# Kernel tuning notes

Measured on AMD Instinct MI355X. Metric: run time of the kernel, lower is better.

Reference implementation:

```python
import jax, jax.numpy as jnp
import numpy as np

N = 50000        # nodes
E = 800000       # edges (avg degree 16)
NODE_D = 128     # node_attr_dim
EDGE_D = 16      # edge_attr_dim
HID = 300        # hidden_dim (module default)


def setup_inputs() -> dict:
    key = jax.random.key(0)
    ks = jax.random.split(key, 8)
    x = jax.random.normal(ks[0], (N, NODE_D), jnp.float32)
    edge_attr = jax.random.normal(ks[1], (E, EDGE_D), jnp.float32)
    edge_weight = jax.random.uniform(ks[2], (E,), jnp.float32)
    node_weight = jax.random.uniform(ks[3], (N,), jnp.float32)
    edge_index = jax.random.randint(ks[4], (2, E), 0, N, jnp.int32)
    # lin0: Linear(node_attr_dim + edge_attr_dim, hidden_dim)
    W0 = jax.random.normal(ks[5], (NODE_D + EDGE_D, HID), jnp.float32) / np.sqrt(NODE_D + EDGE_D)
    b0 = jnp.zeros((HID,), jnp.float32)
    # mp_layer.linear: Linear(hidden_dim, hidden_dim)
    W = jax.random.normal(ks[6], (HID, HID), jnp.float32) / np.sqrt(HID)
    b = jnp.zeros((HID,), jnp.float32)
    return dict(x=x, edge_attr=edge_attr, edge_weight=edge_weight,
                node_weight=node_weight, W0=W0, b0=b0, W=W, b=b,
                edge_index=edge_index)


def reference(x, edge_attr, edge_weight, node_weight, W0, b0, W, b, edge_index):
    src = edge_index[0]   # x_j (source, flow='source_to_target')
    dst = edge_index[1]   # aggregation target i
    n = x.shape[0]

    # --- isFirstLayer: weighted sum of incoming edge features, scattered at dst ---
    inc = jax.ops.segment_sum(edge_weight[:, None] * edge_attr, dst, num_segments=n)  # [N, EDGE_D]
    h0 = jax.nn.relu(jnp.concatenate([x, inc], axis=1) @ W0 + b0)                     # [N, HID]

    # --- MessagePassingLayer: message = edge_weight * x_j; aggr = mean at dst ---
    msg = edge_weight[:, None] * h0[src]                                              # [E, HID]
    agg = jax.ops.segment_sum(msg, dst, num_segments=n)                               # [N, HID]
    deg = jax.ops.segment_sum(jnp.ones((src.shape[0],), x.dtype), dst, num_segments=n)
    agg = agg / jnp.maximum(deg, 1.0)[:, None]  # scatter-mean (0 where no incoming edges)

    # --- update: relu(h0 + linear(aggr)) (add_residual=True) ---
    h = jax.nn.relu(h0 + agg @ W + b)
    # isLastLayer=False -> no node_weight scaling
    return (h, h0)
```

## Files before the change

kernel.cpp:

```cpp
#include <hip/hip_runtime.h>

#define NN 50000
#define NE 800000
#define ND 128
#define ED 16
#define HID 300
#define KP1 192
#define KP2 320
#define NP 320

#define SCAN_T 256
#define SCAN_B ((NN + SCAN_T - 1) / SCAN_T)

typedef __attribute__((ext_vector_type(8))) short short8;
typedef __attribute__((ext_vector_type(4))) float f32x4;

__device__ __forceinline__ unsigned short f2b(float f) {
    unsigned int u = __float_as_uint(f);
    u = (u + 0x7FFFu + ((u >> 16) & 1u)) >> 16;
    return (unsigned short)u;
}
__device__ __forceinline__ float blo(unsigned int u) {
    return __uint_as_float(u << 16);
}
__device__ __forceinline__ float bhi(unsigned int u) {
    return __uint_as_float(u & 0xffff0000u);
}

__device__ __forceinline__ void gload16(const void* g, void* l) {
    __builtin_amdgcn_global_load_lds(
        (const __attribute__((address_space(1))) void*)g,
        (__attribute__((address_space(3))) void*)l, 16, 0, 0);
}

__device__ __forceinline__ int block_iscan(int v, int tid) {
    int lane = tid & 63;
    #pragma unroll
    for (int off = 1; off < 64; off <<= 1) {
        int t = __shfl_up(v, off);
        if (lane >= off) v += t;
    }
    __shared__ int wsum[4];
    int wid = tid >> 6;
    if (lane == 63) wsum[wid] = v;
    __syncthreads();
    int add = 0;
    #pragma unroll
    for (int w = 0; w < 4; ++w)
        if (w < wid) add += wsum[w];
    return v + add;
}

__global__ void hist_kernel(const int* __restrict__ ei, int* __restrict__ rowptr) {
    int e = blockIdx.x * blockDim.x + threadIdx.x;
    if (e < NE) atomicAdd(&rowptr[ei[NE + e] + 1], 1);
}

__global__ __launch_bounds__(SCAN_T) void scan1(int* __restrict__ rowptr,
                                                int* __restrict__ blockSums) {
    int i = blockIdx.x * SCAN_T + threadIdx.x;
    int v = (i < NN) ? rowptr[1 + i] : 0;
    v = block_iscan(v, threadIdx.x);
    if (i < NN) rowptr[1 + i] = v;
    if (threadIdx.x == SCAN_T - 1) blockSums[blockIdx.x] = v;
}

__global__ __launch_bounds__(SCAN_T) void scan2(int* __restrict__ blockSums) {
    int t = threadIdx.x;
    int orig = (t < SCAN_B) ? blockSums[t] : 0;
    int v = block_iscan(orig, t);
    if (t < SCAN_B) blockSums[t] = v - orig;
}

__global__ __launch_bounds__(SCAN_T) void scan3(int* __restrict__ rowptr,
                                                const int* __restrict__ blockSums,
                                                int* __restrict__ cursor) {
    int i = blockIdx.x * SCAN_T + threadIdx.x;
    if (i < NN) {
        int v = rowptr[1 + i] + blockSums[blockIdx.x];
        rowptr[1 + i] = v;
        if (i + 1 < NN) cursor[i + 1] = v;
    }
    if (i == 0) cursor[0] = 0;
}

__global__ void fill_kernel(const int* __restrict__ ei, const float* __restrict__ ew,
                            int* __restrict__ cursor, uint4* __restrict__ csr) {
    int e = blockIdx.x * blockDim.x + threadIdx.x;
    if (e < NE) {
        int d = ei[NE + e];
        int pos = atomicAdd(&cursor[d], 1);
        uint4 q;
        q.x = (unsigned int)ei[e];
        q.y = (unsigned int)e;
        q.z = __float_as_uint(ew[e]);
        q.w = 0;
        csr[pos] = q;
    }
}

__global__ __launch_bounds__(256) void prep_kernel(
    const float* __restrict__ x,
    const float* __restrict__ edge_attr,
    const int* __restrict__ rowptr,
    const uint4* __restrict__ csr,
    unsigned short* __restrict__ A1) {
    int n = (blockIdx.x * blockDim.x + threadIdx.x) >> 6;
    int lane = threadIdx.x & 63;
    if (n >= NN) return;

    float2 v = *(const float2*)&x[(size_t)n * ND + lane * 2];
    unsigned int o = (unsigned int)f2b(v.x) | ((unsigned int)f2b(v.y) << 16);
    *(unsigned int*)&A1[(size_t)n * KP1 + lane * 2] = o;

    int g = lane >> 4, j = lane & 15;
    int lo = rowptr[n], hi = rowptr[n + 1];
    float s = 0.f;
    for (int k = lo + g; k < hi; k += 8) {
        int k1 = (k + 4 < hi) ? k + 4 : k;
        uint4 e0 = csr[k];
        uint4 e1 = csr[k1];
        float a0 = edge_attr[(size_t)e0.y * ED + j];
        float a1 = edge_attr[(size_t)e1.y * ED + j];
        s += __uint_as_float(e0.z) * a0;
        s += ((k + 4 < hi) ? __uint_as_float(e1.z) : 0.f) * a1;
    }
    s += __shfl_xor(s, 16);
    s += __shfl_xor(s, 32);
    if (lane < 16)
        A1[(size_t)n * KP1 + ND + lane] = f2b(s);
    else
        A1[(size_t)n * KP1 + ND + lane] = 0;
}

__global__ void castB0(const float* __restrict__ W0, unsigned short* __restrict__ B0T) {
    int n = blockIdx.x, k = threadIdx.x;
    float v = (n < HID && k < ND + ED) ? W0[(size_t)k * HID + n] : 0.f;
    B0T[(size_t)n * KP1 + k] = f2b(v);
}

__global__ void castB(const float* __restrict__ W, unsigned short* __restrict__ BT) {
    int n = blockIdx.x, k = threadIdx.x;
    float v = (n < HID && k < HID) ? W[(size_t)k * HID + n] : 0.f;
    BT[(size_t)n * KP2 + k] = f2b(v);
}

template <int MODE, int KP, int BN, int WM, int WN, int RPB>
__global__ __launch_bounds__(256) void gemm_stream(
    const unsigned short* __restrict__ A,
    const unsigned short* __restrict__ BT,
    const float* __restrict__ bias,
    const float* __restrict__ RES,
    float* __restrict__ C,
    unsigned short* __restrict__ h0b,
    int M)
{
    constexpr int CPR = KP / 8;
    constexpr int ACH = 32 * CPR;
    constexpr int BCH = BN * CPR;
    constexpr int AM  = 32 / (16 * WM);
    constexpr int BNW = BN / (16 * WN);
    __shared__ unsigned short Bs[BCH * 8];
    __shared__ unsigned short As[2][ACH * 8];

    const int tid = threadIdx.x;
    const int wave = tid >> 6, lane = tid & 63;
    const int wm = wave / WN, wn = wave % WN;
    const int quad = lane >> 4, lr = lane & 15;
    const int n00 = blockIdx.y * BN;
    const int rbase = blockIdx.x * RPB;
    const int rowend = min(rbase + RPB, M);
    const int nt = (rowend - rbase + 31) >> 5;

    #pragma unroll
    for (int rd = 0; rd < BCH / 256; ++rd) {
        int s = rd * 256 + tid;
        int row = s / CPR, c = s - row * CPR;
        int cs = (c & ~7) | ((c & 7) ^ (row & 7));
        gload16(&BT[(size_t)(n00 + row) * KP + cs * 8], &Bs[s * 8]);
    }
    auto stageA = [&](int buf, int mb) {
        #pragma unroll
        for (int rd = 0; rd < ACH / 256; ++rd) {
            int s = rd * 256 + tid;
            int row = s / CPR, c = s - row * CPR;
            int cs = (c & ~7) | ((c & 7) ^ (row & 7));
            int mg = mb + row; if (mg >= M) mg = M - 1;
            gload16(&A[(size_t)mg * KP + cs * 8], &As[buf][s * 8]);
        }
    };
    stageA(0, rbase);

    float bias_r[BNW];
    #pragma unroll
    for (int tn = 0; tn < BNW; ++tn) {
        int ng = n00 + wn * (BNW * 16) + tn * 16 + lr;
        bias_r[tn] = (ng < HID) ? bias[ng] : 0.f;
    }
    __syncthreads();

    int cur = 0;
    #pragma unroll 1
    for (int t = 0; t < nt; ++t) {
        const int mb = rbase + t * 32;
        if (t + 1 < nt) stageA(cur ^ 1, mb + 32);

        float res_r[AM][BNW][4];
        if (MODE == 1) {
            #pragma unroll
            for (int tm = 0; tm < AM; ++tm)
            #pragma unroll
            for (int tn = 0; tn < BNW; ++tn) {
                int ng = n00 + wn * (BNW * 16) + tn * 16 + lr;
                int ngc = ng < HID ? ng : HID - 1;
                #pragma unroll
                for (int r = 0; r < 4; ++r) {
                    int mg = mb + (wm * AM + tm) * 16 + quad * 4 + r;
                    int mgc = mg < M ? mg : M - 1;
                    res_r[tm][tn][r] = RES[(size_t)mgc * HID + ngc];
                }
            }
        }

        f32x4 acc[AM][BNW] = {};
        const int rm = lr & 7;
        #pragma unroll
        for (int tt = 0; tt < KP / 32; ++tt) {
            int cA = tt * 4 + quad;
            int sw8 = ((cA & ~7) | ((cA & 7) ^ rm)) * 8;
            short8 a[AM], b[BNW];
            #pragma unroll
            for (int tm = 0; tm < AM; ++tm) {
                int ar = (wm * AM + tm) * 16 + lr;
                a[tm] = *(const short8*)&As[cur][ar * KP + sw8];
            }
            #pragma unroll
            for (int tn = 0; tn < BNW; ++tn) {
                int br = wn * (BNW * 16) + tn * 16 + lr;
                b[tn] = *(const short8*)&Bs[br * KP + sw8];
            }
            #pragma unroll
            for (int tm = 0; tm < AM; ++tm)
                #pragma unroll
                for (int tn = 0; tn < BNW; ++tn)
                    acc[tm][tn] = __builtin_amdgcn_mfma_f32_16x16x32_bf16(
                        a[tm], b[tn], acc[tm][tn], 0, 0, 0);
        }

        #pragma unroll
        for (int tm = 0; tm < AM; ++tm)
        #pragma unroll
        for (int tn = 0; tn < BNW; ++tn) {
            int ng = n00 + wn * (BNW * 16) + tn * 16 + lr;
            #pragma unroll
            for (int r = 0; r < 4; ++r) {
                int mg = mb + (wm * AM + tm) * 16 + quad * 4 + r;
                if (mg < rowend && ng < HID) {
                    float v = acc[tm][tn][r] + bias_r[tn];
                    if (MODE == 1) v += res_r[tm][tn][r];
                    v = fmaxf(v, 0.f);
                    C[(size_t)mg * HID + ng] = v;
                    if (MODE == 0) h0b[(size_t)mg * NP + ng] = f2b(v);
                }
            }
        }
        __syncthreads();
        cur ^= 1;
    }
}

__device__ __forceinline__ void acc8(float* acc, float w, const uint4& r) {
    acc[0] += w * blo(r.x); acc[1] += w * bhi(r.x);
    acc[2] += w * blo(r.y); acc[3] += w * bhi(r.y);
    acc[4] += w * blo(r.z); acc[5] += w * bhi(r.z);
    acc[6] += w * blo(r.w); acc[7] += w * bhi(r.w);
}

__global__ __launch_bounds__(256) void agg_kernel(
    const unsigned short* __restrict__ h0b,
    const int* __restrict__ rowptr,
    const uint4* __restrict__ csr,
    unsigned short* __restrict__ aggB)
{
    int n = (blockIdx.x * blockDim.x + threadIdx.x) >> 6;
    int lane = threadIdx.x & 63;
    if (n >= NN) return;
    int lo = rowptr[n], hi = rowptr[n + 1];
    float acc[8] = {};
    const uint4* h4 = (const uint4*)h0b;
    bool act = lane < 40;
    for (int k = lo; k < hi; k += 4) {
        int k1 = (k + 1 < hi) ? k + 1 : k;
        int k2 = (k + 2 < hi) ? k + 2 : k;
        int k3 = (k + 3 < hi) ? k + 3 : k;
        uint4 p0 = csr[k], p1 = csr[k1], p2 = csr[k2], p3 = csr[k3];
        float w0 = __uint_as_float(p0.z);
        float w1 = (k + 1 < hi) ? __uint_as_float(p1.z) : 0.f;
        float w2 = (k + 2 < hi) ? __uint_as_float(p2.z) : 0.f;
        float w3 = (k + 3 < hi) ? __uint_as_float(p3.z) : 0.f;
        uint4 r0 = {0,0,0,0}, r1 = {0,0,0,0}, r2 = {0,0,0,0}, r3 = {0,0,0,0};
        if (act) {
            r0 = h4[(size_t)p0.x * 40 + lane];
            r1 = h4[(size_t)p1.x * 40 + lane];
            r2 = h4[(size_t)p2.x * 40 + lane];
            r3 = h4[(size_t)p3.x * 40 + lane];
        }
        acc8(acc, w0, r0);
        acc8(acc, w1, r1);
        acc8(acc, w2, r2);
        acc8(acc, w3, r3);
    }
    if (act) {
        float invd = 1.f / fmaxf((float)(hi - lo), 1.f);
        int cbase = lane * 8;
        unsigned int o[4];
        #pragma unroll
        for (int i = 0; i < 4; ++i) {
            int c0 = cbase + 2 * i, c1 = c0 + 1;
            unsigned int ulo = (c0 < HID) ? f2b(acc[2 * i] * invd) : 0;
            unsigned int uhi = (c1 < HID) ? f2b(acc[2 * i + 1] * invd) : 0;
            o[i] = ulo | (uhi << 16);
        }
        uint4* a4 = (uint4*)aggB;
        uint4 v; v.x = o[0]; v.y = o[1]; v.z = o[2]; v.w = o[3];
        a4[(size_t)n * 40 + lane] = v;
    }
}

extern "C" void kernel_launch(void* const* d_in, const int* in_sizes, int n_in,
                              void* d_out, int out_size, void* d_ws, size_t ws_size,
                              hipStream_t stream) {
    const float* x           = (const float*)d_in[0];
    const float* edge_attr   = (const float*)d_in[1];
    const float* edge_weight = (const float*)d_in[2];
    const float* W0 = (const float*)d_in[4];
    const float* b0 = (const float*)d_in[5];
    const float* W  = (const float*)d_in[6];
    const float* b  = (const float*)d_in[7];
    const int* ei   = (const int*)d_in[8];

    float* out = (float*)d_out;
    float* h  = out;
    float* h0 = out + (size_t)NN * HID;

    char* p = (char*)d_ws;
    auto alloc = [&](size_t bytes) { char* q = p; p += (bytes + 255) & ~(size_t)255; return q; };
    int*   rowptr  = (int*)  alloc((NN + 1) * sizeof(int));
    int*   cursor  = (int*)  alloc(NN * sizeof(int));
    int*   bsums   = (int*)  alloc(SCAN_B * sizeof(int));
    uint4* csr     = (uint4*)alloc((size_t)NE * sizeof(uint4));
    unsigned short* A1   = (unsigned short*)alloc((size_t)NN * KP1 * 2);
    unsigned short* h0b  = (unsigned short*)alloc((size_t)NN * NP * 2);
    unsigned short* aggB = (unsigned short*)alloc((size_t)NN * NP * 2);
    unsigned short* B0T  = (unsigned short*)alloc((size_t)NP * KP1 * 2);
    unsigned short* BT   = (unsigned short*)alloc((size_t)NP * KP2 * 2);

    hipMemsetAsync(rowptr, 0, (NN + 1) * sizeof(int), stream);
    hist_kernel<<<(NE + 255) / 256, 256, 0, stream>>>(ei, rowptr);
    scan1<<<SCAN_B, SCAN_T, 0, stream>>>(rowptr, bsums);
    scan2<<<1, SCAN_T, 0, stream>>>(bsums);
    scan3<<<SCAN_B, SCAN_T, 0, stream>>>(rowptr, bsums, cursor);
    fill_kernel<<<(NE + 255) / 256, 256, 0, stream>>>(ei, edge_weight, cursor, csr);
    castB0<<<NP, KP1, 0, stream>>>(W0, B0T);
    castB<<<NP, KP2, 0, stream>>>(W, BT);
    prep_kernel<<<(NN + 3) / 4, 256, 0, stream>>>(x, edge_attr, rowptr, csr, A1);

    gemm_stream<0, KP1, 320, 1, 4, 196><<<dim3(256, 1), 256, 0, stream>>>(
        A1, B0T, b0, nullptr, h0, h0b, NN);
    agg_kernel<<<(NN + 3) / 4, 256, 0, stream>>>(h0b, rowptr, csr, aggB);
    gemm_stream<1, KP2, 160, 2, 2, 391><<<dim3(128, 2), 256, 0, stream>>>(
        aggB, BT, b, h0, h, nullptr, NN);
}
```

Before: 447.2 us.

## Load GEMM A fragments directly from global, use 512-thread blocks, vectorize histogram

The GEMM kernel drops the double-buffered LDS staging of A tiles and has each wave read its A fragment straight from global memory. Blocks grow to 512 threads (8 waves), each owning 16 rows, and the per-tile __syncthreads is removed. The edge histogram now handles four edges per thread with an int4 load, and the prep kernel unrolls its edge gather by four to expose more memory parallelism. The risk is that uncoalesced direct global A loads without prefetch leave the MFMA loop waiting on memory latency.

```diff
diff --git a/kernel.cpp b/kernel.cpp
--- a/kernel.cpp
+++ b/kernel.cpp
@@ -52,8 +52,14 @@
 }
 
 __global__ void hist_kernel(const int* __restrict__ ei, int* __restrict__ rowptr) {
-    int e = blockIdx.x * blockDim.x + threadIdx.x;
-    if (e < NE) atomicAdd(&rowptr[ei[NE + e] + 1], 1);
+    int e4 = (blockIdx.x * blockDim.x + threadIdx.x) * 4;
+    if (e4 < NE) {
+        int4 d = *(const int4*)&ei[NE + e4];
+        atomicAdd(&rowptr[d.x + 1], 1);
+        atomicAdd(&rowptr[d.y + 1], 1);
+        atomicAdd(&rowptr[d.z + 1], 1);
+        atomicAdd(&rowptr[d.w + 1], 1);
+    }
 }
 
 __global__ __launch_bounds__(SCAN_T) void scan1(int* __restrict__ rowptr,
@@ -116,14 +122,20 @@
     int g = lane >> 4, j = lane & 15;
     int lo = rowptr[n], hi = rowptr[n + 1];
     float s = 0.f;
-    for (int k = lo + g; k < hi; k += 8) {
-        int k1 = (k + 4 < hi) ? k + 4 : k;
-        uint4 e0 = csr[k];
-        uint4 e1 = csr[k1];
+    for (int k = lo + g; k < hi; k += 16) {
+        int k1 = (k + 4  < hi) ? k + 4  : k;
+        int k2 = (k + 8  < hi) ? k + 8  : k;
+        int k3 = (k + 12 < hi) ? k + 12 : k;
+        uint4 e0 = csr[k],  e1 = csr[k1];
+        uint4 e2 = csr[k2], e3 = csr[k3];
         float a0 = edge_attr[(size_t)e0.y * ED + j];
         float a1 = edge_attr[(size_t)e1.y * ED + j];
+        float a2 = edge_attr[(size_t)e2.y * ED + j];
+        float a3 = edge_attr[(size_t)e3.y * ED + j];
         s += __uint_as_float(e0.z) * a0;
-        s += ((k + 4 < hi) ? __uint_as_float(e1.z) : 0.f) * a1;
+        s += ((k + 4  < hi) ? __uint_as_float(e1.z) : 0.f) * a1;
+        s += ((k + 8  < hi) ? __uint_as_float(e2.z) : 0.f) * a2;
+        s += ((k + 12 < hi) ? __uint_as_float(e3.z) : 0.f) * a3;
     }
     s += __shfl_xor(s, 16);
     s += __shfl_xor(s, 32);
@@ -145,8 +157,8 @@
     BT[(size_t)n * KP2 + k] = f2b(v);
 }
 
-template <int MODE, int KP, int BN, int WM, int WN, int RPB>
-__global__ __launch_bounds__(256) void gemm_stream(
+template <int MODE, int KP, int BN, int WM, int WN, int RPB, int TM>
+__global__ __launch_bounds__(512) void gemm_stream(
     const unsigned short* __restrict__ A,
     const unsigned short* __restrict__ BT,
     const float* __restrict__ bias,
@@ -156,116 +168,86 @@
     int M)
 {
     constexpr int CPR = KP / 8;
-    constexpr int ACH = 32 * CPR;
     constexpr int BCH = BN * CPR;
-    constexpr int AM  = 32 / (16 * WM);
     constexpr int BNW = BN / (16 * WN);
-    __shared__ unsigned short Bs[BCH * 8];
-    __shared__ unsigned short As[2][ACH * 8];
+    __shared__ unsigned short Bs[BN * KP];
 
     const int tid = threadIdx.x;
     const int wave = tid >> 6, lane = tid & 63;
     const int wm = wave / WN, wn = wave % WN;
     const int quad = lane >> 4, lr = lane & 15;
     const int n00 = blockIdx.y * BN;
+    const int ncol = n00 + wn * (BNW * 16);
     const int rbase = blockIdx.x * RPB;
     const int rowend = min(rbase + RPB, M);
-    const int nt = (rowend - rbase + 31) >> 5;
-
-    #pragma unroll
-    for (int rd = 0; rd < BCH / 256; ++rd) {
-        int s = rd * 256 + tid;
+    const int nt = (rowend - rbase + TM - 1) / TM;
+
+    for (int s = tid; s < BCH; s += 512) {
         int row = s / CPR, c = s - row * CPR;
         int cs = (c & ~7) | ((c & 7) ^ (row & 7));
         gload16(&BT[(size_t)(n00 + row) * KP + cs * 8], &Bs[s * 8]);
     }
-    auto stageA = [&](int buf, int mb) {
-        #pragma unroll
-        for (int rd = 0; rd < ACH / 256; ++rd) {
-            int s = rd * 256 + tid;
-            int row = s / CPR, c = s - row * CPR;
-            int cs = (c & ~7) | ((c & 7) ^ (row & 7));
-            int mg = mb + row; if (mg >= M) mg = M - 1;
-            gload16(&A[(size_t)mg * KP + cs * 8], &As[buf][s * 8]);
-        }
-    };
-    stageA(0, rbase);
-
     float bias_r[BNW];
     #pragma unroll
     for (int tn = 0; tn < BNW; ++tn) {
-        int ng = n00 + wn * (BNW * 16) + tn * 16 + lr;
+        int ng = ncol + tn * 16 + lr;
         bias_r[tn] = (ng < HID) ? bias[ng] : 0.f;
     }
     __syncthreads();
 
-    int cur = 0;
     #pragma unroll 1
     for (int t = 0; t < nt; ++t) {
-        const int mb = rbase + t * 32;
-        if (t + 1 < nt) stageA(cur ^ 1, mb + 32);
-
-        float res_r[AM][BNW][4];
+        const int mb = rbase + t * TM;
+        int arow = mb + wm * 16 + lr; if (arow >= M) arow = M - 1;
+        const unsigned short* ap = A + (size_t)arow * KP;
+
+        float res_r[BNW][4];
         if (MODE == 1) {
             #pragma unroll
-            for (int tm = 0; tm < AM; ++tm)
-            #pragma unroll
             for (int tn = 0; tn < BNW; ++tn) {
-                int ng = n00 + wn * (BNW * 16) + tn * 16 + lr;
+                int ng = ncol + tn * 16 + lr;
                 int ngc = ng < HID ? ng : HID - 1;
                 #pragma unroll
                 for (int r = 0; r < 4; ++r) {
-                    int mg = mb + (wm * AM + tm) * 16 + quad * 4 + r;
+                    int mg = mb + wm * 16 + quad * 4 + r;
                     int mgc = mg < M ? mg : M - 1;
-                    res_r[tm][tn][r] = RES[(size_t)mgc * HID + ngc];
+                    res_r[tn][r] = RES[(size_t)mgc * HID + ngc];
                 }
             }
         }
 
-        f32x4 acc[AM][BNW] = {};
+        f32x4 acc[BNW] = {};
         const int rm = lr & 7;
         #pragma unroll
         for (int tt = 0; tt < KP / 32; ++tt) {
-            int cA = tt * 4 + quad;
-            int sw8 = ((cA & ~7) | ((cA & 7) ^ rm)) * 8;
-            short8 a[AM], b[BNW];
+            short8 a = *(const short8*)&ap[tt * 32 + quad * 8];
+            int cB = tt * 4 + quad;
+            int sw8 = ((cB & ~7) | ((cB & 7) ^ rm)) * 8;
+            short8 b[BNW];
             #pragma unroll
-            for (int tm = 0; tm < AM; ++tm) {
-                int ar = (wm * AM + tm) * 16 + lr;
-                a[tm] = *(const short8*)&As[cur][ar * KP + sw8];
-            }
+            for (int tn = 0; tn < BNW; ++tn)
+                b[tn] = *(const short8*)&Bs[(wn * (BNW * 16) + tn * 16 + lr) * KP + sw8];
             #pragma unroll
-            for (int tn = 0; tn < BNW; ++tn) {
-                int br = wn * (BNW * 16) + tn * 16 + lr;
-                b[tn] = *(const short8*)&Bs[br * KP + sw8];
-            }
-            #pragma unroll
-            for (int tm = 0; tm < AM; ++tm)
-                #pragma unroll
-                for (int tn = 0; tn < BNW; ++tn)
-                    acc[tm][tn] = __builtin_amdgcn_mfma_f32_16x16x32_bf16(
-                        a[tm], b[tn], acc[tm][tn], 0, 0, 0);
-        }
-
-        #pragma unroll
-        for (int tm = 0; tm < AM; ++tm)
+            for (int tn = 0; tn < BNW; ++tn)
+                acc[tn] = __builtin_amdgcn_mfma_f32_16x16x32_bf16(
+                    a, b[tn], acc[tn], 0, 0, 0);
+        }
+
         #pragma unroll
         for (int tn = 0; tn < BNW; ++tn) {
-            int ng = n00 + wn * (BNW * 16) + tn * 16 + lr;
+            int ng = ncol + tn * 16 + lr;
             #pragma unroll
             for (int r = 0; r < 4; ++r) {
-                int mg = mb + (wm * AM + tm) * 16 + quad * 4 + r;
+                int mg = mb + wm * 16 + quad * 4 + r;
                 if (mg < rowend && ng < HID) {
-                    float v = acc[tm][tn][r] + bias_r[tn];
-                    if (MODE == 1) v += res_r[tm][tn][r];
+                    float v = acc[tn][r] + bias_r[tn];
+                    if (MODE == 1) v += res_r[tn][r];
                     v = fmaxf(v, 0.f);
                     C[(size_t)mg * HID + ng] = v;
                     if (MODE == 0) h0b[(size_t)mg * NP + ng] = f2b(v);
                 }
             }
         }
-        __syncthreads();
-        cur ^= 1;
     }
 }
 
@@ -356,7 +338,7 @@
     unsigned short* BT   = (unsigned short*)alloc((size_t)NP * KP2 * 2);
 
     hipMemsetAsync(rowptr, 0, (NN + 1) * sizeof(int), stream);
-    hist_kernel<<<(NE + 255) / 256, 256, 0, stream>>>(ei, rowptr);
+    hist_kernel<<<(NE / 4 + 255) / 256, 256, 0, stream>>>(ei, rowptr);
     scan1<<<SCAN_B, SCAN_T, 0, stream>>>(rowptr, bsums);
     scan2<<<1, SCAN_T, 0, stream>>>(bsums);
     scan3<<<SCAN_B, SCAN_T, 0, stream>>>(rowptr, bsums, cursor);
@@ -365,9 +347,9 @@
     castB<<<NP, KP2, 0, stream>>>(W, BT);
     prep_kernel<<<(NN + 3) / 4, 256, 0, stream>>>(x, edge_attr, rowptr, csr, A1);
 
-    gemm_stream<0, KP1, 320, 1, 4, 196><<<dim3(256, 1), 256, 0, stream>>>(
+    gemm_stream<0, KP1, 320, 2, 4, 196, 32><<<dim3(256, 1), 512, 0, stream>>>(
         A1, B0T, b0, nullptr, h0, h0b, NN);
     agg_kernel<<<(NN + 3) / 4, 256, 0, stream>>>(h0b, rowptr, csr, aggB);
-    gemm_stream<1, KP2, 160, 2, 2, 391><<<dim3(128, 2), 256, 0, stream>>>(
+    gemm_stream<1, KP2, 160, 4, 2, 391, 64><<<dim3(128, 2), 512, 0, stream>>>(
         aggB, BT, b, h0, h, nullptr, NN);
 }
```

Result: slower. 471.1 us (+5.4%).
